# Performance work log

Hardware: AMD Instinct MI355X
Metric: run time of the kernel (lower is better)

The kernel has to match this reference:

```python
import jax, jax.numpy as jnp
import numpy as np

N = 4194304          # pixels (e.g. 2048x2048 render)
MOTION = 8
H = 8
OUT = 3
N_LAYERS = 3
Z_SCALE = 10.0
INV_SQRT_2PI = 1.0 / np.sqrt(2.0 * np.pi)

# activation set chosen from Fun.funs: sin, gaus, tanh, id
FUNS = [
    jnp.sin,
    lambda t: INV_SQRT_2PI * jnp.exp(-0.5 * t * t),  # 'gaus'
    jnp.tanh,
    lambda t: t,                                      # 'id'
]


def _make_masks(rng):
    # mirror __init__: per layer, permute H cells and split into len(Funs) sorted groups
    masks = []
    for _ in range(N_LAYERS):
        perm = rng.permutation(H)
        masks.append([np.sort(a) for a in np.array_split(perm, len(FUNS))])
    return jnp.asarray(np.array(masks), dtype=jnp.int64)  # [L, F, H/F]


def setup_inputs() -> dict:
    key = jax.random.key(0)
    ks = jax.random.split(key, 10)
    rng = np.random.default_rng(0)
    return {
        "x": jax.random.normal(ks[0], (N, 1), jnp.float32),
        "y": jax.random.normal(ks[1], (N, 1), jnp.float32),
        "r": jax.random.uniform(ks[2], (N, 1), jnp.float32),
        "z": jax.random.normal(ks[3], (N, MOTION), jnp.float32),
        "W0": jax.random.normal(ks[4], (H, MOTION + 3), jnp.float32) * 0.3,
        "b0": jax.random.normal(ks[5], (H,), jnp.float32) * 0.1,
        "Wm": jax.random.normal(ks[6], (H, H), jnp.float32) * 0.3,
        "bm": jax.random.normal(ks[7], (H,), jnp.float32) * 0.1,
        "Wo": jax.random.normal(ks[8], (OUT, H), jnp.float32) * 0.3,
        "bo": jax.random.normal(ks[9], (OUT,), jnp.float32) * 0.1,
        "masks": _make_masks(rng),
    }


def reference(x, y, r, z, W0, b0, Wm, bm, Wo, bo, masks):
    inp = jnp.concatenate([z / Z_SCALE, x, y, r], axis=1)  # [N, MOTION+3]
    out = inp @ W0.T + b0                                  # [N, H]
    for l in range(N_LAYERS):
        # NOTE: original repeats the same Linear module -> shared Wm/bm across layers
        pre = out @ Wm.T + bm
        new_out = jnp.zeros_like(out)
        for f, fn in enumerate(FUNS):
            m = masks[l, f]                                # disjoint column group
            new_out = new_out.at[:, m].set(fn(pre[:, m]))
        out = (new_out + out) * 0.5
    return jax.nn.sigmoid(out @ Wo.T + bo)                 # [N, OUT]
```

## Files before the change

### kernel.cpp

```cpp
#include <hip/hip_runtime.h>


__global__ void cppn_prep(const float* __restrict__ W0,
                          const float* __restrict__ b0,
                          const float* __restrict__ Wm,
                          const float* __restrict__ bm,
                          const float* __restrict__ Wo,
                          const float* __restrict__ bo,
                          const int* __restrict__ masks,
                          float* __restrict__ wf,
                          int* __restrict__ wi) {
    int t = threadIdx.x;
    if (t < 88) {
        int k = t % 11;
        wf[t] = W0[t] * (k < 8 ? 0.1f : 1.0f);
    } else if (t < 96) {
        wf[t] = b0[t - 88];
    } else if (t < 160) {
        wf[t] = Wm[t - 96];
    } else if (t < 168) {
        wf[t] = bm[t - 160];
    } else if (t < 192) {
        wf[t] = Wo[t - 168];
    } else if (t < 195) {
        wf[t] = bo[t - 192];
    } else if (t < 195 + 24) {
        int j = t - 195;
        bool is64 = true;
        for (int q = 1; q < 24; q += 2) is64 = is64 && (masks[q] == 0);
        int c = is64 ? masks[2 * j] : masks[j];
        int l = j >> 3;
        int f = (j & 7) >> 1;
        wi[256 + l * 8 + c] = f;
    }
}

__global__ __launch_bounds__(256) void cppn_main(
    const float* __restrict__ xb,
    const float* __restrict__ yb,
    const float* __restrict__ rb,
    const float4* __restrict__ zb,
    const float* __restrict__ wf,
    const int* __restrict__ fid,
    float* __restrict__ out,
    int n) {
    int i = blockIdx.x * 256 + threadIdx.x;
    if (i >= n) return;

    float4 z0 = zb[2 * i];
    float4 z1 = zb[2 * i + 1];
    float in[11];
    in[0] = z0.x; in[1] = z0.y; in[2] = z0.z; in[3] = z0.w;
    in[4] = z1.x; in[5] = z1.y; in[6] = z1.z; in[7] = z1.w;
    in[8]  = xb[i];
    in[9]  = yb[i];
    in[10] = rb[i];

    float o[8];
#pragma unroll
    for (int h = 0; h < 8; ++h) {
        float acc = wf[88 + h];
#pragma unroll
        for (int k = 0; k < 11; ++k)
            acc = fmaf(wf[h * 11 + k], in[k], acc);
        o[h] = acc;
    }

#pragma unroll
    for (int l = 0; l < 3; ++l) {
        float p[8];
#pragma unroll
        for (int h = 0; h < 8; ++h) {
            float acc = wf[160 + h];
#pragma unroll
            for (int k = 0; k < 8; ++k)
                acc = fmaf(wf[96 + h * 8 + k], o[k], acc);
            p[h] = acc;
        }
#pragma unroll
        for (int h = 0; h < 8; ++h) {
            int f = __builtin_amdgcn_readfirstlane(fid[l * 8 + h]);
            float t = p[h];
            float v;
            if (f == 0) {
                v = __sinf(t);
            } else if (f == 1) {
                v = 0.3989422804014327f * __expf(-0.5f * t * t);
            } else if (f == 2) {
                float e = __expf(2.0f * t);
                v = 1.0f - 2.0f * __builtin_amdgcn_rcpf(e + 1.0f);
            } else {
                v = t;
            }
            o[h] = 0.5f * (v + o[h]);
        }
    }

#pragma unroll
    for (int j = 0; j < 3; ++j) {
        float acc = wf[192 + j];
#pragma unroll
        for (int k = 0; k < 8; ++k)
            acc = fmaf(wf[168 + j * 8 + k], o[k], acc);
        float e = __expf(-acc);
        out[3 * i + j] = __builtin_amdgcn_rcpf(1.0f + e);
    }
}

extern "C" void kernel_launch(void* const* d_in, const int* in_sizes, int n_in,
                              void* d_out, int out_size, void* d_ws, size_t ws_size,
                              hipStream_t stream) {
    const float* xb = (const float*)d_in[0];
    const float* yb = (const float*)d_in[1];
    const float* rb = (const float*)d_in[2];
    const float* zb = (const float*)d_in[3];
    const float* W0 = (const float*)d_in[4];
    const float* b0 = (const float*)d_in[5];
    const float* Wm = (const float*)d_in[6];
    const float* bm = (const float*)d_in[7];
    const float* Wo = (const float*)d_in[8];
    const float* bo = (const float*)d_in[9];
    const int* masks = (const int*)d_in[10];

    float* wf = (float*)d_ws;
    int*   wi = (int*)d_ws;

    int n = in_sizes[0];

    cppn_prep<<<1, 256, 0, stream>>>(W0, b0, Wm, bm, Wo, bo, masks, wf, wi);
    cppn_main<<<(n + 255) / 256, 256, 0, stream>>>(
        xb, yb, rb, (const float4*)zb, wf, wi + 256,
        (float*)d_out, n);
}
```

Baseline: 259.3 us.

## Process two pixels per thread and fold averaging scale into weights

Each thread now handles two pixels so that the uniform weight loads and the readfirstlane activation dispatch are shared across both. The per-layer 0.5 averaging is replaced by an unnormalized accumulator: the layer weights are prescaled by 1, 0.5 and 0.25, the output weights by 0.125, and the update becomes a single FMA with scale 1, 2 or 4. This removes a multiply per unit per layer and amortizes scalar loads, at the cost of higher register pressure and half as many blocks.

```diff
diff --git a/kernel.cpp b/kernel.cpp
--- a/kernel.cpp
+++ b/kernel.cpp
@@ -16,24 +16,29 @@
         wf[t] = W0[t] * (k < 8 ? 0.1f : 1.0f);
     } else if (t < 96) {
         wf[t] = b0[t - 88];
-    } else if (t < 160) {
-        wf[t] = Wm[t - 96];
-    } else if (t < 168) {
-        wf[t] = bm[t - 160];
-    } else if (t < 192) {
-        wf[t] = Wo[t - 168];
-    } else if (t < 195) {
-        wf[t] = bo[t - 192];
-    } else if (t < 195 + 24) {
-        int j = t - 195;
+    } else if (t < 288) {
+        int j = t - 96;
+        int l = j >> 6;
+        float s = (l == 0) ? 1.0f : (l == 1 ? 0.5f : 0.25f);
+        wf[96 + j] = Wm[j & 63] * s;
+    } else if (t < 296) {
+        wf[t] = bm[t - 288];
+    } else if (t < 320) {
+        wf[t] = Wo[t - 296] * 0.125f;
+    } else if (t < 323) {
+        wf[t] = bo[t - 320];
+    } else if (t < 323 + 24) {
+        int j = t - 323;
         bool is64 = true;
         for (int q = 1; q < 24; q += 2) is64 = is64 && (masks[q] == 0);
         int c = is64 ? masks[2 * j] : masks[j];
         int l = j >> 3;
         int f = (j & 7) >> 1;
-        wi[256 + l * 8 + c] = f;
+        wi[384 + l * 8 + c] = f;
     }
 }
+
+#define PX 2
 
 __global__ __launch_bounds__(256) void cppn_main(
     const float* __restrict__ xb,
@@ -44,66 +49,98 @@
     const int* __restrict__ fid,
     float* __restrict__ out,
     int n) {
-    int i = blockIdx.x * 256 + threadIdx.x;
-    if (i >= n) return;
+    int base = blockIdx.x * (256 * PX) + threadIdx.x;
+    int idx[PX];
+    bool ok[PX];
+#pragma unroll
+    for (int px = 0; px < PX; ++px) {
+        idx[px] = base + px * 256;
+        ok[px] = idx[px] < n;
+    }
 
-    float4 z0 = zb[2 * i];
-    float4 z1 = zb[2 * i + 1];
-    float in[11];
-    in[0] = z0.x; in[1] = z0.y; in[2] = z0.z; in[3] = z0.w;
-    in[4] = z1.x; in[5] = z1.y; in[6] = z1.z; in[7] = z1.w;
-    in[8]  = xb[i];
-    in[9]  = yb[i];
-    in[10] = rb[i];
+    float in[PX][11];
+#pragma unroll
+    for (int px = 0; px < PX; ++px) {
+        int i = ok[px] ? idx[px] : 0;
+        float4 z0 = zb[2 * i];
+        float4 z1 = zb[2 * i + 1];
+        in[px][0] = z0.x; in[px][1] = z0.y; in[px][2] = z0.z; in[px][3] = z0.w;
+        in[px][4] = z1.x; in[px][5] = z1.y; in[px][6] = z1.z; in[px][7] = z1.w;
+        in[px][8]  = xb[i];
+        in[px][9]  = yb[i];
+        in[px][10] = rb[i];
+    }
 
-    float o[8];
+    float u[PX][8];
 #pragma unroll
     for (int h = 0; h < 8; ++h) {
-        float acc = wf[88 + h];
 #pragma unroll
-        for (int k = 0; k < 11; ++k)
-            acc = fmaf(wf[h * 11 + k], in[k], acc);
-        o[h] = acc;
+        for (int px = 0; px < PX; ++px) {
+            float acc = wf[88 + h];
+#pragma unroll
+            for (int k = 0; k < 11; ++k)
+                acc = fmaf(wf[h * 11 + k], in[px][k], acc);
+            u[px][h] = acc;
+        }
     }
 
 #pragma unroll
     for (int l = 0; l < 3; ++l) {
-        float p[8];
+        const float* W = wf + 96 + 64 * l;
+        const float scale = (l == 0) ? 1.0f : (l == 1 ? 2.0f : 4.0f);
+        float p[PX][8];
 #pragma unroll
         for (int h = 0; h < 8; ++h) {
-            float acc = wf[160 + h];
 #pragma unroll
-            for (int k = 0; k < 8; ++k)
-                acc = fmaf(wf[96 + h * 8 + k], o[k], acc);
-            p[h] = acc;
+            for (int px = 0; px < PX; ++px) {
+                float acc = wf[288 + h];
+#pragma unroll
+                for (int k = 0; k < 8; ++k)
+                    acc = fmaf(W[h * 8 + k], u[px][k], acc);
+                p[px][h] = acc;
+            }
         }
 #pragma unroll
         for (int h = 0; h < 8; ++h) {
             int f = __builtin_amdgcn_readfirstlane(fid[l * 8 + h]);
-            float t = p[h];
-            float v;
+            float v[PX];
             if (f == 0) {
-                v = __sinf(t);
+#pragma unroll
+                for (int px = 0; px < PX; ++px) v[px] = __sinf(p[px][h]);
             } else if (f == 1) {
-                v = 0.3989422804014327f * __expf(-0.5f * t * t);
+#pragma unroll
+                for (int px = 0; px < PX; ++px) {
+                    float t = p[px][h];
+                    v[px] = 0.3989422804014327f * __expf(-0.5f * t * t);
+                }
             } else if (f == 2) {
-                float e = __expf(2.0f * t);
-                v = 1.0f - 2.0f * __builtin_amdgcn_rcpf(e + 1.0f);
+#pragma unroll
+                for (int px = 0; px < PX; ++px) {
+                    float e = __expf(2.0f * p[px][h]);
+                    v[px] = fmaf(-2.0f, __builtin_amdgcn_rcpf(e + 1.0f), 1.0f);
+                }
             } else {
-                v = t;
+#pragma unroll
+                for (int px = 0; px < PX; ++px) v[px] = p[px][h];
             }
-            o[h] = 0.5f * (v + o[h]);
+#pragma unroll
+            for (int px = 0; px < PX; ++px)
+                u[px][h] = fmaf(scale, v[px], u[px][h]);
         }
     }
 
 #pragma unroll
     for (int j = 0; j < 3; ++j) {
-        float acc = wf[192 + j];
 #pragma unroll
-        for (int k = 0; k < 8; ++k)
-            acc = fmaf(wf[168 + j * 8 + k], o[k], acc);
-        float e = __expf(-acc);
-        out[3 * i + j] = __builtin_amdgcn_rcpf(1.0f + e);
+        for (int px = 0; px < PX; ++px) {
+            float acc = wf[320 + j];
+#pragma unroll
+            for (int k = 0; k < 8; ++k)
+                acc = fmaf(wf[296 + j * 8 + k], u[px][k], acc);
+            float e = __expf(-acc);
+            float v = __builtin_amdgcn_rcpf(1.0f + e);
+            if (ok[px]) out[3 * idx[px] + j] = v;
+        }
     }
 }
 
@@ -127,8 +164,9 @@
 
     int n = in_sizes[0];
 
-    cppn_prep<<<1, 256, 0, stream>>>(W0, b0, Wm, bm, Wo, bo, masks, wf, wi);
-    cppn_main<<<(n + 255) / 256, 256, 0, stream>>>(
-        xb, yb, rb, (const float4*)zb, wf, wi + 256,
+    cppn_prep<<<1, 512, 0, stream>>>(W0, b0, Wm, bm, Wo, bo, masks, wf, wi);
+    int per_block = 256 * PX;
+    cppn_main<<<(n + per_block - 1) / per_block, 256, 0, stream>>>(
+        xb, yb, rb, (const float4*)zb, wf, wi + 384,
         (float*)d_out, n);
 }
```

Measured after the change: 258.8 us. About the same (-0.2%).
